# Optimization experiments

Hardware: AMD Instinct MI355X
Metric: run time of the kernel (lower is better)

## Reference

```python
import jax, jax.numpy as jnp
import numpy as np

T, B, H = 512, 128, 512

def setup_inputs() -> dict:
    key = jax.random.key(0)
    k1, k2, k3, k4 = jax.random.split(key, 4)
    s = 1.0 / np.sqrt(H)
    x = jax.random.normal(k1, (T, B, H), dtype=jnp.float32)
    resets = jax.random.randint(k2, (T, B), 0, 2).astype(bool)
    Wi = jax.random.normal(k3, (H, 3 * H), dtype=jnp.float32) * s
    bi = jnp.zeros((3 * H,), dtype=jnp.float32)
    Wh = jax.random.normal(k4, (H, 3 * H), dtype=jnp.float32) * s
    bhn = jnp.zeros((H,), dtype=jnp.float32)
    h0 = jnp.zeros((B, H), dtype=jnp.float32)
    return {"x": x, "resets": resets, "Wi": Wi, "bi": bi, "Wh": Wh, "bhn": bhn, "h0": h0}

def reference(x, resets, Wi, bi, Wh, bhn, h0):
    # Scanned flax GRUCell with per-step carry reset (reset -> zeros carry).
    def step(h, inp):
        xt, rt = inp                                   # xt: [B,H], rt: [B]
        h = jnp.where(rt[:, None], jnp.zeros_like(h), h)
        gi = xt @ Wi + bi                              # [B,3H]
        gh = h @ Wh                                    # [B,3H]
        ir, iz, inn = jnp.split(gi, 3, axis=-1)
        hr, hz, hn = jnp.split(gh, 3, axis=-1)
        r = jax.nn.sigmoid(ir + hr)
        z = jax.nn.sigmoid(iz + hz)
        n = jnp.tanh(inn + r * (hn + bhn))             # bias only on h 'n' gate (flax GRUCell)
        new_h = (1.0 - z) * n + z * h
        return new_h, new_h
    _, ys = jax.lax.scan(step, h0, (x, resets))
    return ys                                          # [T,B,H]
```

## Files before the change

kernel.cpp:

```cpp
#include <hip/hip_runtime.h>


typedef _Float16 f16;
typedef _Float16 f16x8 __attribute__((ext_vector_type(8)));
typedef float f32x4 __attribute__((ext_vector_type(4)));

#define TT 512
#define BB 128
#define HH 512
#define H3 1536
#define TBR 65536
#define NC 64
#define CL 8
#define NR 8192
static const size_t PL = (size_t)TBR * HH;

__device__ __forceinline__ float sigf(float x) { return 1.f / (1.f + __expf(-x)); }

__global__ __launch_bounds__(256) void k_prep(
    const float* __restrict__ Wi, const float* __restrict__ Wh,
    const int* __restrict__ resets,
    f16* __restrict__ WiT, f16* __restrict__ WhT,
    int* __restrict__ fr, int* __restrict__ cnt) {
  int idx = blockIdx.x * 256 + threadIdx.x;
  if (idx < HH * H3) {
    int n = idx >> 9;
    int k = idx & (HH - 1);
    WiT[idx] = (f16)Wi[(size_t)k * H3 + n];
    WhT[idx] = (f16)Wh[(size_t)k * H3 + n];
  }
  if (idx < NR) {
    int c = idx >> 7, b = idx & 127;
    int f = CL;
    for (int s = CL - 1; s >= 0; --s)
      if (resets[(c * CL + s) * BB + b]) f = s;
    fr[idx] = f;
    atomicAdd(&cnt[f], 1);
  }
}

__global__ void k_sort(int* __restrict__ cnt) {
  int st = 0;
  cnt[16 + 8] = 0;
  for (int f = 7; f >= 0; --f) {
    st += cnt[f + 1];
    cnt[16 + f] = st;
  }
  for (int f = 1; f <= 8; ++f) cnt[32 + f] = cnt[16 + f];
}

__global__ __launch_bounds__(256) void k_scatter(
    const int* __restrict__ fr, int* __restrict__ cnt, int* __restrict__ list) {
  int idx = blockIdx.x * 256 + threadIdx.x;
  if (idx < NR) {
    int f = fr[idx];
    if (f >= 1) {
      int pos = atomicAdd(&cnt[32 + f], 1);
      list[pos] = idx;
    }
  }
}

__global__ __launch_bounds__(256) void k_gemm_gi(
    const float* __restrict__ x, const f16* __restrict__ WiT,
    const float* __restrict__ bi, f16* __restrict__ gi) {
  __shared__ __align__(16) f16 As[64 * 48];
  __shared__ __align__(16) f16 Bs[64 * 48];
  const int tid = threadIdx.x;
  const int lane = tid & 63;
  const int w = tid >> 6;
  const int i0 = blockIdx.x * 64;
  const int j0 = blockIdx.y * 64;
  const int mw = (w & 1) * 32;
  const int nw = (w >> 1) * 32;

  f32x4 acc[2][2] = {};
  const int srow = tid >> 2;
  const int skp = (tid & 3) * 8;
  const int fr = lane & 15;
  const int fq8 = (lane >> 4) * 8;

  for (int kb = 0; kb < 16; ++kb) {
    const int k0 = kb * 32;
    const float* xp = x + (size_t)(i0 + srow) * HH + k0 + skp;
    float4 v0 = *(const float4*)xp;
    float4 v1 = *(const float4*)(xp + 4);
    f16x8 a8;
    a8[0] = (f16)v0.x; a8[1] = (f16)v0.y; a8[2] = (f16)v0.z; a8[3] = (f16)v0.w;
    a8[4] = (f16)v1.x; a8[5] = (f16)v1.y; a8[6] = (f16)v1.z; a8[7] = (f16)v1.w;
    *(f16x8*)&As[srow * 48 + skp] = a8;
    *(f16x8*)&Bs[srow * 48 + skp] =
        *(const f16x8*)(WiT + (size_t)(j0 + srow) * HH + k0 + skp);
    __syncthreads();
    f16x8 af0 = *(const f16x8*)&As[(mw + fr) * 48 + fq8];
    f16x8 af1 = *(const f16x8*)&As[(mw + 16 + fr) * 48 + fq8];
    f16x8 bf0 = *(const f16x8*)&Bs[(nw + fr) * 48 + fq8];
    f16x8 bf1 = *(const f16x8*)&Bs[(nw + 16 + fr) * 48 + fq8];
    acc[0][0] = __builtin_amdgcn_mfma_f32_16x16x32_f16(af0, bf0, acc[0][0], 0, 0, 0);
    acc[0][1] = __builtin_amdgcn_mfma_f32_16x16x32_f16(af0, bf1, acc[0][1], 0, 0, 0);
    acc[1][0] = __builtin_amdgcn_mfma_f32_16x16x32_f16(af1, bf0, acc[1][0], 0, 0, 0);
    acc[1][1] = __builtin_amdgcn_mfma_f32_16x16x32_f16(af1, bf1, acc[1][1], 0, 0, 0);
    __syncthreads();
  }
  const int trow = (lane >> 4) * 4;
  for (int mi = 0; mi < 2; ++mi)
    for (int ni = 0; ni < 2; ++ni)
      for (int r = 0; r < 4; ++r) {
        int row = mw + mi * 16 + trow + r;
        int col = nw + ni * 16 + fr;
        int j = j0 + col;
        int p = j >> 9, jj = j & 511;
        gi[(size_t)p * PL + (size_t)(i0 + row) * HH + jj] =
            (f16)(acc[mi][ni][r] + bi[j]);
      }
}

__global__ __launch_bounds__(256) void k_step0(
    const int* __restrict__ resets, const f16* __restrict__ gi,
    const float* __restrict__ bhn, float* __restrict__ out,
    f16* __restrict__ hA) {
  int gid = blockIdx.x * 256 + threadIdx.x;
  int row = gid >> 6;
  int c8 = (gid & 63) * 8;
  int c = row >> 7, b = row & 127;
  size_t girow = (size_t)c * 1024 + b;
  const f16x8 g0 = *(const f16x8*)(gi + girow * HH + c8);
  const f16x8 g1 = *(const f16x8*)(gi + PL + girow * HH + c8);
  const f16x8 g2 = *(const f16x8*)(gi + 2 * PL + girow * HH + c8);
  const int z1 = resets[(c * CL + 1) * BB + b];
  float4 o[2];
  f16x8 hn;
#pragma unroll
  for (int u = 0; u < 8; ++u) {
    float r = sigf((float)g0[u]);
    float z = sigf((float)g1[u]);
    float n = tanhf((float)g2[u] + r * bhn[c8 + u]);
    float h = (1.f - z) * n;
    ((float*)o)[u] = h;
    hn[u] = z1 ? (f16)0.f : (f16)h;
  }
  *(float4*)(out + girow * HH + c8) = o[0];
  *(float4*)(out + girow * HH + c8 + 4) = o[1];
  *(f16x8*)(hA + (size_t)row * HH + c8) = hn;
}

__global__ __launch_bounds__(256, 2) void k_phase1(
    int s, const int* __restrict__ resets, const f16* __restrict__ WhT,
    const f16* __restrict__ gi, const float* __restrict__ bhn,
    float* __restrict__ out, const f16* __restrict__ hrd,
    f16* __restrict__ hwr) {
  __shared__ __align__(16) f16 As[128 * 40];
  __shared__ __align__(16) f16 Bs[192 * 40];
  const int tid = threadIdx.x;
  const int lane = tid & 63;
  const int w = tid >> 6;
  const int c = blockIdx.x;
  const int j0 = blockIdx.y * 64;
  const int t = c * CL + s;
  const int wm = (w & 1) * 64;
  const int wn = (w >> 1) * 32;
  const int fr = lane & 15;
  const int q8 = (lane >> 4) * 8;

  f32x4 acc[3][4][2] = {};

  for (int kb = 0; kb < 16; ++kb) {
    const int k0 = kb * 32;
#pragma unroll
    for (int uu = 0; uu < 2; ++uu) {
      int u = tid + uu * 256;
      int row = u >> 2, oc = (u & 3) * 8;
      *(f16x8*)&As[row * 40 + oc] =
          *(const f16x8*)(hrd + ((size_t)(c * BB + row)) * HH + k0 + oc);
    }
#pragma unroll
    for (int uu = 0; uu < 3; ++uu) {
      int u = tid + uu * 256;
      int row = u >> 2, oc = (u & 3) * 8;
      int g = row >> 6, j = j0 + (row & 63);
      *(f16x8*)&Bs[row * 40 + oc] =
          *(const f16x8*)(WhT + ((size_t)(g * HH + j)) * HH + k0 + oc);
    }
    __syncthreads();
    f16x8 af[4];
#pragma unroll
    for (int mi = 0; mi < 4; ++mi)
      af[mi] = *(const f16x8*)&As[(wm + mi * 16 + fr) * 40 + q8];
    f16x8 bf[3][2];
#pragma unroll
    for (int g = 0; g < 3; ++g)
#pragma unroll
      for (int ni = 0; ni < 2; ++ni)
        bf[g][ni] = *(const f16x8*)&Bs[(g * 64 + wn + ni * 16 + fr) * 40 + q8];
#pragma unroll
    for (int g = 0; g < 3; ++g)
#pragma unroll
      for (int mi = 0; mi < 4; ++mi)
#pragma unroll
        for (int ni = 0; ni < 2; ++ni)
          acc[g][mi][ni] = __builtin_amdgcn_mfma_f32_16x16x32_f16(
              af[mi], bf[g][ni], acc[g][mi][ni], 0, 0, 0);
    __syncthreads();
  }

  const int trow = (lane >> 4) * 4;
#pragma unroll
  for (int mi = 0; mi < 4; ++mi)
#pragma unroll
    for (int ni = 0; ni < 2; ++ni) {
      const int j = j0 + wn + ni * 16 + fr;
      const float bh = bhn[j];
#pragma unroll
      for (int r = 0; r < 4; ++r) {
        const int b = wm + mi * 16 + trow + r;
        const size_t girow = (size_t)c * 1024 + (size_t)s * BB + b;
        const float gr = (float)gi[girow * HH + j];
        const float gz = (float)gi[PL + girow * HH + j];
        const float gn = (float)gi[2 * PL + girow * HH + j];
        const float hp = (float)hrd[((size_t)(c * BB + b)) * HH + j];
        const float rr = sigf(gr + acc[0][mi][ni][r]);
        const float zz = sigf(gz + acc[1][mi][ni][r]);
        const float nn = tanhf(gn + rr * (acc[2][mi][ni][r] + bh));
        const float hnew = (1.f - zz) * nn + zz * hp;
        out[girow * HH + j] = hnew;
        int zr = (s < 7) ? resets[(t + 1) * BB + b] : 0;
        hwr[((size_t)(c * BB + b)) * HH + j] = zr ? (f16)0.f : (f16)hnew;
      }
    }
}

__global__ __launch_bounds__(256) void k_bound(
    const int* __restrict__ fr, const f16* __restrict__ hend,
    const float* __restrict__ h0, f16* __restrict__ hin) {
  int gid = blockIdx.x * 256 + threadIdx.x;
  int row = gid >> 6;
  int o8 = (gid & 63) * 8;
  int c = row >> 7, b = row & 127;
  if (c == 0) {
    const float* hp = h0 + (size_t)b * HH + o8;
    float4 v0 = *(const float4*)hp;
    float4 v1 = *(const float4*)(hp + 4);
    f16x8 h;
    h[0] = (f16)v0.x; h[1] = (f16)v0.y; h[2] = (f16)v0.z; h[3] = (f16)v0.w;
    h[4] = (f16)v1.x; h[5] = (f16)v1.y; h[6] = (f16)v1.z; h[7] = (f16)v1.w;
    *(f16x8*)(hin + (size_t)row * HH + o8) = h;
  } else if (fr[row - BB] < CL) {
    *(f16x8*)(hin + (size_t)row * HH + o8) =
        *(const f16x8*)(hend + (size_t)(row - BB) * HH + o8);
  }
}

__global__ __launch_bounds__(1024) void k_chain(
    const int* __restrict__ fr, const f16* __restrict__ hend,
    const f16* __restrict__ WhT, const f16* __restrict__ gi,
    const float* __restrict__ bhn, const float* __restrict__ h0,
    f16* __restrict__ hin) {
  const int row0 = blockIdx.x;
  const int c0 = row0 >> 7, b = row0 & 127;
  if (fr[row0] != CL) return;
  if (c0 > 0 && fr[row0 - BB] == CL) return;
  if (c0 == NC - 1) return;

  __shared__ float hs[HH];
  __shared__ float gh[H3];
  __shared__ float part[8 * H3];
  const int tid = threadIdx.x;
  const int lane = tid & 63;
  const int w = tid >> 6;
  if (c0 == 0) {
    for (int i = tid; i < HH; i += 1024) hs[i] = h0[(size_t)b * HH + i];
  } else {
    for (int i = tid; i < HH; i += 1024)
      hs[i] = (float)hend[(size_t)(row0 - BB) * HH + i];
  }
  __syncthreads();

  int c = c0;
  while (c < NC - 1) {
    for (int s = 0; s < CL; ++s) {
      const size_t girow = (size_t)(c * CL + s) * BB + b;
      float gr_v = 0.f, gz_v = 0.f, gn_v = 0.f, hp_v = 0.f, bh_v = 0.f;
      if (tid < HH) {
        gr_v = (float)gi[girow * HH + tid];
        gz_v = (float)gi[PL + girow * HH + tid];
        gn_v = (float)gi[2 * PL + girow * HH + tid];
        bh_v = bhn[tid];
        hp_v = hs[tid];
      }
      float hv[8];
      {
        float4 h0v = *(const float4*)&hs[lane * 8];
        float4 h1v = *(const float4*)&hs[lane * 8 + 4];
        hv[0] = h0v.x; hv[1] = h0v.y; hv[2] = h0v.z; hv[3] = h0v.w;
        hv[4] = h1v.x; hv[5] = h1v.y; hv[6] = h1v.z; hv[7] = h1v.w;
      }
      const f16* wp = WhT + (size_t)(w * 96) * HH + lane * 8;
#pragma unroll 8
      for (int r = 0; r < 96; ++r) {
        f16x8 wv = *(const f16x8*)(wp + (size_t)r * HH);
        float a = 0.f;
#pragma unroll
        for (int u = 0; u < 8; ++u) a += (float)wv[u] * hv[u];
        a += __shfl_xor(a, 32, 64);
        a += __shfl_xor(a, 16, 64);
        a += __shfl_xor(a, 8, 64);
        if (lane < 8) part[lane * H3 + (w * 96 + r)] = a;
      }
      __syncthreads();
      for (int n = tid; n < H3; n += 1024) {
        float a = part[n];
#pragma unroll
        for (int u = 1; u < 8; ++u) a += part[u * H3 + n];
        gh[n] = a;
      }
      __syncthreads();
      if (tid < HH) {
        const int j = tid;
        const float rr = sigf(gr_v + gh[j]);
        const float zz = sigf(gz_v + gh[HH + j]);
        const float nn = tanhf(gn_v + rr * (gh[2 * HH + j] + bh_v));
        hs[j] = (1.f - zz) * nn + zz * hp_v;
      }
      __syncthreads();
    }
    const int nrow = (c + 1) * BB + b;
    for (int i = tid; i < HH; i += 1024)
      hin[(size_t)nrow * HH + i] = (f16)hs[i];
    if (fr[nrow] != CL) break;
    ++c;
  }
}

__global__ __launch_bounds__(256) void k_phase3(
    int s, const int* __restrict__ cnt, const int* __restrict__ list,
    const f16* __restrict__ WhT, const f16* __restrict__ gi,
    const float* __restrict__ bhn, float* __restrict__ out,
    f16* __restrict__ hph) {
  const int count = cnt[16 + s];
  const int r0 = blockIdx.x * 16;
  if (r0 >= count) return;
  __shared__ __align__(16) f16 As[16 * 520];
  __shared__ int rows[16];
  const int tid = threadIdx.x;
  const int lane = tid & 63;
  const int w = tid >> 6;
  if (tid < 16) rows[tid] = (r0 + tid < count) ? list[r0 + tid] : -1;
  __syncthreads();
#pragma unroll
  for (int uu = 0; uu < 4; ++uu) {
    int u = tid + uu * 256;
    int row = u >> 6, oc = (u & 63) * 8;
    int rid = rows[row];
    f16x8 v = {};
    if (rid >= 0) v = *(const f16x8*)(hph + (size_t)rid * HH + oc);
    *(f16x8*)&As[row * 520 + oc] = v;
  }
  __syncthreads();
  const int fr16 = lane & 15;
  const int q8 = (lane >> 4) * 8;
  const int trow = (lane >> 4) * 4;
  for (int jt = 0; jt < 8; ++jt) {
    const int jb = w * 128 + jt * 16;
    f32x4 a0 = {}, a1 = {}, a2 = {};
#pragma unroll 4
    for (int kb = 0; kb < 16; ++kb) {
      const int k0 = kb * 32;
      f16x8 af = *(const f16x8*)&As[fr16 * 520 + k0 + q8];
      f16x8 b0 = *(const f16x8*)(WhT + ((size_t)(jb + fr16)) * HH + k0 + q8);
      f16x8 b1 = *(const f16x8*)(WhT + ((size_t)(HH + jb + fr16)) * HH + k0 + q8);
      f16x8 b2 = *(const f16x8*)(WhT + ((size_t)(2 * HH + jb + fr16)) * HH + k0 + q8);
      a0 = __builtin_amdgcn_mfma_f32_16x16x32_f16(af, b0, a0, 0, 0, 0);
      a1 = __builtin_amdgcn_mfma_f32_16x16x32_f16(af, b1, a1, 0, 0, 0);
      a2 = __builtin_amdgcn_mfma_f32_16x16x32_f16(af, b2, a2, 0, 0, 0);
    }
    const int j = jb + fr16;
    const float bh = bhn[j];
#pragma unroll
    for (int r = 0; r < 4; ++r) {
      const int rid = rows[trow + r];
      if (rid < 0) continue;
      const int c = rid >> 7, b = rid & 127;
      const size_t girow = (size_t)(c * CL + s) * BB + b;
      const float gr = (float)gi[girow * HH + j];
      const float gz = (float)gi[PL + girow * HH + j];
      const float gn = (float)gi[2 * PL + girow * HH + j];
      const float hp = (float)hph[(size_t)rid * HH + j];
      const float rr = sigf(gr + a0[r]);
      const float zz = sigf(gz + a1[r]);
      const float nn = tanhf(gn + rr * (a2[r] + bh));
      const float hnew = (1.f - zz) * nn + zz * hp;
      out[girow * HH + j] = hnew;
      hph[(size_t)rid * HH + j] = (f16)hnew;
    }
  }
}

extern "C" void kernel_launch(void* const* d_in, const int* in_sizes, int n_in,
                              void* d_out, int out_size, void* d_ws, size_t ws_size,
                              hipStream_t stream) {
  const float* x = (const float*)d_in[0];
  const int* resets = (const int*)d_in[1];
  const float* Wi = (const float*)d_in[2];
  const float* bi = (const float*)d_in[3];
  const float* Wh = (const float*)d_in[4];
  const float* bhn = (const float*)d_in[5];
  const float* h0 = (const float*)d_in[6];
  float* out = (float*)d_out;

  char* ws = (char*)d_ws;
  size_t off = 0;
  f16* gi = (f16*)(ws + off);   off += 3 * PL * sizeof(f16);
  f16* WiT = (f16*)(ws + off);  off += (size_t)HH * H3 * sizeof(f16);
  f16* WhT = (f16*)(ws + off);  off += (size_t)HH * H3 * sizeof(f16);
  f16* hA = (f16*)(ws + off);   off += (size_t)NR * HH * sizeof(f16);
  f16* hB = (f16*)(ws + off);   off += (size_t)NR * HH * sizeof(f16);
  f16* hin = (f16*)(ws + off);  off += (size_t)NR * HH * sizeof(f16);
  int* fr = (int*)(ws + off);   off += NR * sizeof(int);
  int* list = (int*)(ws + off); off += NR * sizeof(int);
  int* cnt = (int*)(ws + off);  off += 64 * sizeof(int);
  (void)ws_size; (void)in_sizes; (void)n_in; (void)out_size;

  hipMemsetAsync(cnt, 0, 64 * sizeof(int), stream);
  k_prep<<<dim3(3072), 256, 0, stream>>>(Wi, Wh, resets, WiT, WhT, fr, cnt);
  k_sort<<<dim3(1), 1, 0, stream>>>(cnt);
  k_scatter<<<dim3(32), 256, 0, stream>>>(fr, cnt, list);
  k_gemm_gi<<<dim3(TBR / 64, H3 / 64), 256, 0, stream>>>(x, WiT, bi, gi);
  k_step0<<<dim3(NR * 64 / 256), 256, 0, stream>>>(resets, gi, bhn, out, hA);
  for (int s = 1; s < CL; ++s) {
    const f16* hrd = (s & 1) ? hA : hB;
    f16* hwr = (s & 1) ? hB : hA;
    k_phase1<<<dim3(NC, 8), 256, 0, stream>>>(s, resets, WhT, gi, bhn, out, hrd, hwr);
  }
  k_bound<<<dim3(NR * 64 / 256), 256, 0, stream>>>(fr, hB, h0, hin);
  k_chain<<<dim3(NR), 1024, 0, stream>>>(fr, hB, WhT, gi, bhn, h0, hin);
  for (int s = 0; s < CL; ++s)
    k_phase3<<<dim3(NR / 16), 256, 0, stream>>>(s, cnt, list, WhT, gi, bhn, out, hin);
}
```

Measured before the change: 2.045 ms.

## Restructure input GEMM: stage full x row-tile in LDS, loop over all columns

The input projection GEMM now loads and converts a 64-row tile of x to fp16 once into 64KB of shared memory in an MFMA-friendly layout. It then loops over all 1536 output columns per block, using 32x32x16 MFMAs with weights read directly from global memory. Previously each 64x64 output tile re-read and re-converted x, 24 times over, and synchronised every k-step. The trade-offs are fewer blocks with larger LDS use, which lowers occupancy, and weight fragments fetched from global or L2 without LDS sharing.

```diff
diff --git a/kernel.cpp b/kernel.cpp
--- a/kernel.cpp
+++ b/kernel.cpp
@@ -4,6 +4,7 @@
 typedef _Float16 f16;
 typedef _Float16 f16x8 __attribute__((ext_vector_type(8)));
 typedef float f32x4 __attribute__((ext_vector_type(4)));
+typedef float f32x16 __attribute__((ext_vector_type(16)));
 
 #define TT 512
 #define BB 128
@@ -64,55 +65,66 @@
 __global__ __launch_bounds__(256) void k_gemm_gi(
     const float* __restrict__ x, const f16* __restrict__ WiT,
     const float* __restrict__ bi, f16* __restrict__ gi) {
-  __shared__ __align__(16) f16 As[64 * 48];
-  __shared__ __align__(16) f16 Bs[64 * 48];
+  __shared__ __align__(16) f16 xs[64 * 512];
   const int tid = threadIdx.x;
   const int lane = tid & 63;
   const int w = tid >> 6;
-  const int i0 = blockIdx.x * 64;
-  const int j0 = blockIdx.y * 64;
-  const int mw = (w & 1) * 32;
-  const int nw = (w >> 1) * 32;
-
-  f32x4 acc[2][2] = {};
-  const int srow = tid >> 2;
-  const int skp = (tid & 3) * 8;
-  const int fr = lane & 15;
-  const int fq8 = (lane >> 4) * 8;
-
-  for (int kb = 0; kb < 16; ++kb) {
-    const int k0 = kb * 32;
-    const float* xp = x + (size_t)(i0 + srow) * HH + k0 + skp;
-    float4 v0 = *(const float4*)xp;
-    float4 v1 = *(const float4*)(xp + 4);
-    f16x8 a8;
-    a8[0] = (f16)v0.x; a8[1] = (f16)v0.y; a8[2] = (f16)v0.z; a8[3] = (f16)v0.w;
-    a8[4] = (f16)v1.x; a8[5] = (f16)v1.y; a8[6] = (f16)v1.z; a8[7] = (f16)v1.w;
-    *(f16x8*)&As[srow * 48 + skp] = a8;
-    *(f16x8*)&Bs[srow * 48 + skp] =
-        *(const f16x8*)(WiT + (size_t)(j0 + srow) * HH + k0 + skp);
-    __syncthreads();
-    f16x8 af0 = *(const f16x8*)&As[(mw + fr) * 48 + fq8];
-    f16x8 af1 = *(const f16x8*)&As[(mw + 16 + fr) * 48 + fq8];
-    f16x8 bf0 = *(const f16x8*)&Bs[(nw + fr) * 48 + fq8];
-    f16x8 bf1 = *(const f16x8*)&Bs[(nw + 16 + fr) * 48 + fq8];
-    acc[0][0] = __builtin_amdgcn_mfma_f32_16x16x32_f16(af0, bf0, acc[0][0], 0, 0, 0);
-    acc[0][1] = __builtin_amdgcn_mfma_f32_16x16x32_f16(af0, bf1, acc[0][1], 0, 0, 0);
-    acc[1][0] = __builtin_amdgcn_mfma_f32_16x16x32_f16(af1, bf0, acc[1][0], 0, 0, 0);
-    acc[1][1] = __builtin_amdgcn_mfma_f32_16x16x32_f16(af1, bf1, acc[1][1], 0, 0, 0);
-    __syncthreads();
-  }
-  const int trow = (lane >> 4) * 4;
-  for (int mi = 0; mi < 2; ++mi)
-    for (int ni = 0; ni < 2; ++ni)
-      for (int r = 0; r < 4; ++r) {
-        int row = mw + mi * 16 + trow + r;
-        int col = nw + ni * 16 + fr;
-        int j = j0 + col;
-        int p = j >> 9, jj = j & 511;
-        gi[(size_t)p * PL + (size_t)(i0 + row) * HH + jj] =
-            (f16)(acc[mi][ni][r] + bi[j]);
-      }
+  const size_t i0 = (size_t)blockIdx.x * 64;
+
+  {
+    const int row = tid >> 2;
+    const int mi = row >> 5;
+    const int lin = (row & 31) + ((tid & 1) << 5);
+    const int koct = (tid & 3) * 8;
+#pragma unroll 4
+    for (int kb32 = 0; kb32 < 16; ++kb32) {
+      const int k = kb32 * 32 + koct;
+      const float* xp = x + (i0 + row) * HH + k;
+      float4 v0 = *(const float4*)xp;
+      float4 v1 = *(const float4*)(xp + 4);
+      f16x8 a8;
+      a8[0] = (f16)v0.x; a8[1] = (f16)v0.y; a8[2] = (f16)v0.z; a8[3] = (f16)v0.w;
+      a8[4] = (f16)v1.x; a8[5] = (f16)v1.y; a8[6] = (f16)v1.z; a8[7] = (f16)v1.w;
+      *(f16x8*)&xs[((k >> 4) * 2 + mi) * 512 + lin * 8] = a8;
+    }
+  }
+  __syncthreads();
+
+  const int ln31 = lane & 31;
+  const int kh8 = (lane >> 5) * 8;
+  const int r4 = (lane >> 5) * 4;
+
+  for (int jt = 0; jt < 6; ++jt) {
+    const int j0 = jt * 256 + w * 64;
+    f32x16 acc[2][2] = {};
+    const f16* bp0 = WiT + (size_t)(j0 + ln31) * HH + kh8;
+    const f16* bp1 = bp0 + (size_t)32 * HH;
+#pragma unroll 4
+    for (int kb = 0; kb < 32; ++kb) {
+      f16x8 af0 = *(const f16x8*)&xs[(kb * 2 + 0) * 512 + lane * 8];
+      f16x8 af1 = *(const f16x8*)&xs[(kb * 2 + 1) * 512 + lane * 8];
+      f16x8 bf0 = *(const f16x8*)(bp0 + kb * 16);
+      f16x8 bf1 = *(const f16x8*)(bp1 + kb * 16);
+      acc[0][0] = __builtin_amdgcn_mfma_f32_32x32x16_f16(af0, bf0, acc[0][0], 0, 0, 0);
+      acc[0][1] = __builtin_amdgcn_mfma_f32_32x32x16_f16(af0, bf1, acc[0][1], 0, 0, 0);
+      acc[1][0] = __builtin_amdgcn_mfma_f32_32x32x16_f16(af1, bf0, acc[1][0], 0, 0, 0);
+      acc[1][1] = __builtin_amdgcn_mfma_f32_32x32x16_f16(af1, bf1, acc[1][1], 0, 0, 0);
+    }
+#pragma unroll
+    for (int ni = 0; ni < 2; ++ni) {
+      const int j = j0 + ni * 32 + ln31;
+      const float bj = bi[j];
+      const int p = j >> 9, jj = j & 511;
+#pragma unroll
+      for (int mi = 0; mi < 2; ++mi)
+#pragma unroll
+        for (int r = 0; r < 16; ++r) {
+          const int row = mi * 32 + (r & 3) + 8 * (r >> 2) + r4;
+          gi[(size_t)p * PL + (i0 + row) * HH + jj] =
+              (f16)(acc[mi][ni][r] + bj);
+        }
+    }
+  }
 }
 
 __global__ __launch_bounds__(256) void k_step0(
@@ -424,7 +436,7 @@
   k_prep<<<dim3(3072), 256, 0, stream>>>(Wi, Wh, resets, WiT, WhT, fr, cnt);
   k_sort<<<dim3(1), 1, 0, stream>>>(cnt);
   k_scatter<<<dim3(32), 256, 0, stream>>>(fr, cnt, list);
-  k_gemm_gi<<<dim3(TBR / 64, H3 / 64), 256, 0, stream>>>(x, WiT, bi, gi);
+  k_gemm_gi<<<dim3(TBR / 64), 256, 0, stream>>>(x, WiT, bi, gi);
   k_step0<<<dim3(NR * 64 / 256), 256, 0, stream>>>(resets, gi, bhn, out, hA);
   for (int s = 1; s < CL; ++s) {
     const f16* hrd = (s & 1) ? hA : hB;
```

Result: faster. 1.848 ms (-9.6%).
